# Kernel optimization log

Hardware: AMD Instinct MI355X
Metric: run time of the kernel (lower is better)

Reference implementation:

```python
import jax, jax.numpy as jnp
import numpy as np

IN_F = 512
OUT_F = 512
ALPHA = 0.2  # LeakyReLU negative slope
# dropout p=0.1 is a no-op at inference (training=False), so omitted


def setup_inputs() -> dict:
    key = jax.random.key(0)
    k1, k2, k3 = jax.random.split(key, 3)
    B, N = 16, 1024
    x = jax.random.normal(k1, (B, N, IN_F), dtype=jnp.float32)
    # xavier_uniform with gain=1.414
    limW = 1.414 * np.sqrt(6.0 / (IN_F + OUT_F))
    W = jax.random.uniform(k2, (IN_F, OUT_F), minval=-limW, maxval=limW, dtype=jnp.float32)
    lima = 1.414 * np.sqrt(6.0 / (2 * OUT_F + 1))
    a = jax.random.uniform(k3, (2 * OUT_F, 1), minval=-lima, maxval=lima, dtype=jnp.float32)
    beta = jnp.ones((1,), dtype=jnp.float32)
    return {"x": x, "W": W, "a": a, "beta": beta}


def reference(x, W, a, beta):
    # h: [B, N, F]
    h = jnp.matmul(x, W)
    # Split attention vector: e_ij = leakyrelu(h_i . a1 + h_j . a2)
    a1 = a[:OUT_F, 0]   # [F]
    a2 = a[OUT_F:, 0]   # [F]
    s1 = jnp.einsum('bnf,f->bn', h, a1)  # [B, N]
    s2 = jnp.einsum('bnf,f->bn', h, a2)  # [B, N]
    e = s1[:, :, None] + s2[:, None, :]  # [B, N, N]
    e = jnp.where(e > 0, e, ALPHA * e)   # LeakyReLU
    attention = jax.nn.softmax(e, axis=2)
    h_prime = jnp.einsum('bnm,bmf->bnf', attention, h)
    out = jax.nn.elu(h_prime + beta * h)
    return out
```

## Files before the change

kernel.cpp:

```cpp
#include <hip/hip_runtime.h>

using u16 = unsigned short;
using u32 = unsigned int;

#define ALPHA 0.2f
#define LOG2E 1.4426950408889634f

typedef __bf16 bf16x8 __attribute__((ext_vector_type(8)));
typedef float f32x4 __attribute__((ext_vector_type(4)));
typedef float f32x16 __attribute__((ext_vector_type(16)));

__device__ __forceinline__ u16 f2bf(float f) {
  u32 u = __builtin_bit_cast(u32, f);
  u += 0x7FFFu + ((u >> 16) & 1u);
  return (u16)(u >> 16);
}
__device__ __forceinline__ float bf2f(u16 h) {
  u32 u = ((u32)h) << 16;
  return __builtin_bit_cast(float, u);
}
__device__ __forceinline__ void gload_lds16(const void* g, void* l) {
  __builtin_amdgcn_global_load_lds((__attribute__((address_space(1))) void*)g,
                                   (__attribute__((address_space(3))) void*)l,
                                   16, 0, 0);
}

__global__ __launch_bounds__(256) void k_cast_wT(const float* __restrict__ W, u16* __restrict__ wbt) {
  int idx = blockIdx.x * 256 + threadIdx.x;
  int k = idx >> 9, n = idx & 511;
  wbt[n * 512 + k] = f2bf(W[idx]);
}


__global__ __launch_bounds__(256, 2) void k_gemm1(const float* __restrict__ x, const u16* __restrict__ wbt,
                                                  const float* __restrict__ a,
                                                  u16* __restrict__ hbf, u16* __restrict__ hbt2,
                                                  float* __restrict__ s1p, float* __restrict__ s2p) {
  __shared__ __attribute__((aligned(16))) char lds[73728];
  __shared__ __attribute__((aligned(16))) float a_l[256];

  const int t = threadIdx.x;
  const int lane = t & 63;
  const int w = t >> 6;
  const int l31 = lane & 31, lhi = lane >> 5;
  const int rb = w >> 1, cg = w & 1;
  const int g = blockIdx.x;
  const int cb = (g >> 3) & 3;
  const int tile_m = (g & 7) | ((g >> 5) << 3);
  const int row0 = tile_m * 128;
  const int col0 = cb * 128;

  a_l[t] = (t < 128) ? a[col0 + t] : a[512 + col0 + (t - 128)];

  f32x16 acc[2][2];
#pragma unroll
  for (int i = 0; i < 2; ++i)
#pragma unroll
    for (int j = 0; j < 2; ++j)
#pragma unroll
      for (int r = 0; r < 16; ++r) acc[i][j][r] = 0.f;

#define STAGE_G1(kt, Ab, Bb)                                                              \
  {                                                                                       \
    const int k0_ = (kt) * 32;                                                            \
    _Pragma("unroll")                                                                     \
    for (int i = 0; i < 4; ++i) {                                                         \
      int G = i * 256 + t;                                                                \
      int row = G >> 3, ks = G & 7;                                                       \
      gload_lds16(x + (size_t)(row0 + row) * 512 + k0_ + ((ks ^ (row & 7)) * 4),          \
                  (Ab) + (size_t)(i * 256 + w * 64) * 16);                                \
    }                                                                                     \
    _Pragma("unroll")                                                                     \
    for (int i = 0; i < 2; ++i) {                                                         \
      int G = i * 256 + t;                                                                \
      int col = G >> 2, ks = G & 3;                                                       \
      gload_lds16(wbt + (size_t)(col0 + col) * 512 + k0_ + ((ks ^ ((col >> 1) & 3)) * 8), \
                  (Bb) + (size_t)(i * 256 + w * 64) * 16);                                \
    }                                                                                     \
  }

#define COMPUTE_G1(Ab, Bb)                                                                         \
  {                                                                                                \
    _Pragma("unroll")                                                                              \
    for (int ks = 0; ks < 2; ++ks) {                                                               \
      bf16x8 af[2];                                                                                \
      _Pragma("unroll")                                                                            \
      for (int sub = 0; sub < 2; ++sub) {                                                          \
        const int arow = rb * 64 + sub * 32 + l31;                                                 \
        const int kg = ks * 4 + lhi * 2;                                                           \
        f32x4 fa0 = *reinterpret_cast<const f32x4*>((Ab) + (size_t)(arow * 8 + (kg ^ (arow & 7))) * 16); \
        f32x4 fa1 = *reinterpret_cast<const f32x4*>((Ab) + (size_t)(arow * 8 + ((kg + 1) ^ (arow & 7))) * 16); \
        _Pragma("unroll")                                                                          \
        for (int jj = 0; jj < 4; ++jj) {                                                           \
          af[sub][jj] = (__bf16)fa0[jj];                                                           \
          af[sub][jj + 4] = (__bf16)fa1[jj];                                                       \
        }                                                                                          \
      }                                                                                            \
      bf16x8 bfr[2];                                                                               \
      _Pragma("unroll")                                                                            \
      for (int bt = 0; bt < 2; ++bt) {                                                             \
        const int bcol = cg * 64 + bt * 32 + l31;                                                  \
        const int kslot = (ks * 2 + lhi) ^ ((bcol >> 1) & 3);                                      \
        bfr[bt] = *reinterpret_cast<const bf16x8*>((Bb) + (size_t)(bcol * 4 + kslot) * 16);        \
      }                                                                                            \
      _Pragma("unroll")                                                                            \
      for (int sub = 0; sub < 2; ++sub)                                                            \
        _Pragma("unroll")                                                                          \
        for (int bt = 0; bt < 2; ++bt)                                                             \
          acc[sub][bt] = __builtin_amdgcn_mfma_f32_32x32x16_bf16(af[sub], bfr[bt], acc[sub][bt], 0, 0, 0); \
    }                                                                                              \
  }

  char* Ac = lds;             char* Bc = lds + 49152;
  char* An = lds + 16384;     char* Bn = lds + 57344;
  char* As = lds + 32768;     char* Bs = lds + 65536;

  STAGE_G1(0, Ac, Bc);
  STAGE_G1(1, An, Bn);
  __builtin_amdgcn_sched_barrier(0);
  asm volatile("s_waitcnt vmcnt(6) lgkmcnt(0)" ::: "memory");
  __builtin_amdgcn_s_barrier();
  __builtin_amdgcn_sched_barrier(0);

#pragma unroll 1
  for (int kt = 0; kt < 14; ++kt) {
    STAGE_G1(kt + 2, As, Bs);
    COMPUTE_G1(Ac, Bc);
    __builtin_amdgcn_sched_barrier(0);
    asm volatile("s_waitcnt vmcnt(6)" ::: "memory");
    __builtin_amdgcn_s_barrier();
    __builtin_amdgcn_sched_barrier(0);
    char* ta = Ac; Ac = An; An = As; As = ta;
    char* tb = Bc; Bc = Bn; Bn = Bs; Bs = tb;
  }
  COMPUTE_G1(Ac, Bc);
  __builtin_amdgcn_sched_barrier(0);
  asm volatile("s_waitcnt vmcnt(0)" ::: "memory");
  __builtin_amdgcn_s_barrier();
  __builtin_amdgcn_sched_barrier(0);
  COMPUTE_G1(An, Bn);
#undef STAGE_G1
#undef COMPUTE_G1

  __syncthreads();

  u16* lT = (u16*)lds;
#pragma unroll
  for (int sub = 0; sub < 2; ++sub)
#pragma unroll
    for (int bt = 0; bt < 2; ++bt) {
      const int col = cg * 64 + bt * 32 + l31;
#pragma unroll
      for (int r = 0; r < 16; ++r) {
        int row = rb * 64 + sub * 32 + (r & 3) + 8 * (r >> 2) + 4 * lhi;
        lT[row * 136 + col] = f2bf(acc[sub][bt][r]);
      }
    }
  __syncthreads();

#pragma unroll
  for (int i = 0; i < 8; ++i) {
    int G = i * 256 + t;
    int row = G >> 4, gg = G & 15;
    uint4 v = *reinterpret_cast<const uint4*>(&lT[row * 136 + gg * 8]);
    *reinterpret_cast<uint4*>(&hbf[(size_t)(row0 + row) * 512 + col0 + gg * 8]) = v;
  }
  const int bb = row0 >> 10;
  const int nb = row0 & 1023;
  u16* hb2 = hbt2 + (size_t)bb * 524288;
#pragma unroll
  for (int i = 0; i < 8; ++i) {
    int G = i * 256 + t;
    int col = G & 127, rg = G >> 7;
    u32 wd[4];
#pragma unroll
    for (int jj = 0; jj < 4; ++jj) {
      u16 lo = lT[(rg * 8 + 2 * jj) * 136 + col];
      u16 hi = lT[(rg * 8 + 2 * jj + 1) * 136 + col];
      wd[jj] = (u32)lo | ((u32)hi << 16);
    }
    uint4 o = {wd[0], wd[1], wd[2], wd[3]};
    const int m0 = nb + rg * 8;
    const int f = col0 + col;
    size_t idx = (size_t)(m0 >> 4) * 8192 + (size_t)(f >> 5) * 512 + (size_t)((m0 >> 3) & 1) * 256 + (size_t)(f & 31) * 8;
    *reinterpret_cast<uint4*>(&hb2[idx]) = o;
  }
  {
    const int r2 = t >> 1, half = t & 1;
    float d1 = 0.f, d2 = 0.f;
#pragma unroll
    for (int i = 0; i < 8; ++i) {
      uint4 v = *reinterpret_cast<const uint4*>(&lT[r2 * 136 + half * 64 + i * 8]);
      u32 wds[4] = {v.x, v.y, v.z, v.w};
#pragma unroll
      for (int jj = 0; jj < 8; ++jj) {
        float h = bf2f((u16)(wds[jj >> 1] >> ((jj & 1) * 16)));
        d1 += h * a_l[half * 64 + i * 8 + jj];
        d2 += h * a_l[128 + half * 64 + i * 8 + jj];
      }
    }
    d1 += __shfl_xor(d1, 1);
    d2 += __shfl_xor(d2, 1);
    if (half == 0) {
      s1p[cb * 16384 + row0 + r2] = d1;
      s2p[cb * 16384 + row0 + r2] = d2;
    }
  }
}

__global__ __launch_bounds__(256) void k_reduce(const float* __restrict__ s1p, const float* __restrict__ s2p,
                                                float* __restrict__ s1L, float* __restrict__ s2L) {
  int id = blockIdx.x * 256 + threadIdx.x;
  float d1 = s1p[id] + s1p[16384 + id] + s1p[32768 + id] + s1p[49152 + id];
  float d2 = s2p[id] + s2p[16384 + id] + s2p[32768 + id] + s2p[49152 + id];
  s1L[id] = d1 * LOG2E;
  s2L[id] = d2 * LOG2E;
}

__global__ __launch_bounds__(256, 2) void k_attn(const u16* __restrict__ hbt2, const u16* __restrict__ hbf,
                                                 const float* __restrict__ s1Lg, const float* __restrict__ s2Lg,
                                                 const float* __restrict__ betag, float* __restrict__ out) {
  __shared__ __attribute__((aligned(16))) float e1_l[1024];
  __shared__ __attribute__((aligned(16))) float e2_l[1024];
  __shared__ __attribute__((aligned(16))) float inv_l[128];
  const int t = threadIdx.x;
  const int lane = t & 63;
  const int w = t >> 6;
  const int l31 = lane & 31, lhi = lane >> 5;

  const int B = blockIdx.x;
  const int b = (B & 7) * 2 + ((B >> 3) & 1);
  const int j = B >> 4;
  const int n0 = (j >> 2) * 128;
  const int c0 = (j & 3) * 128;

  const u16* hb2 = hbt2 + (size_t)b * 524288;

  for (int i = t; i < 1024; i += 256) {
    float v = s2Lg[b * 1024 + i];
    e1_l[i] = exp2f(v);
    e2_l[i] = exp2f(ALPHA * v);
  }

  const int myrow = n0 + w * 32 + l31;
  const float s1v = s1Lg[b * 1024 + myrow];
  const float c1 = exp2f(s1v), c2 = exp2f(ALPHA * s1v);

  f32x16 acc[4];
#pragma unroll
  for (int ct = 0; ct < 4; ++ct)
#pragma unroll
    for (int r = 0; r < 16; ++r) acc[ct][r] = 0.f;
  float psum = 0.f;

  __syncthreads();

  const u16* bp = hb2 + (size_t)(c0 >> 5) * 512 + (size_t)(lhi * 32 + l31) * 8;

#define STEP_ATTN(s, buf)                                                      \
  {                                                                            \
    const int mo = (s) * 16 + lhi * 8;                                         \
    f32x4 ea = *reinterpret_cast<const f32x4*>(&e1_l[mo]);                     \
    f32x4 eb = *reinterpret_cast<const f32x4*>(&e1_l[mo + 4]);                 \
    f32x4 fa = *reinterpret_cast<const f32x4*>(&e2_l[mo]);                     \
    f32x4 fb = *reinterpret_cast<const f32x4*>(&e2_l[mo + 4]);                 \
    bf16x8 af;                                                                 \
    _Pragma("unroll")                                                          \
    for (int q = 0; q < 4; ++q) {                                              \
      float p0 = fmaxf(c1 * ea[q], c2 * fa[q]);                                \
      float p1 = fmaxf(c1 * eb[q], c2 * fb[q]);                                \
      psum += p0 + p1;                                                         \
      af[q] = (__bf16)p0;                                                      \
      af[q + 4] = (__bf16)p1;                                                  \
    }                                                                          \
    _Pragma("unroll")                                                          \
    for (int ct = 0; ct < 4; ++ct)                                             \
      acc[ct] = __builtin_amdgcn_mfma_f32_32x32x16_bf16(af, (buf)[ct], acc[ct], 0, 0, 0); \
  }

  bf16x8 bv[4];
#pragma unroll
  for (int ct = 0; ct < 4; ++ct) bv[ct] = *reinterpret_cast<const bf16x8*>(bp + ct * 512);

#pragma unroll 4
  for (int s = 0; s < 63; ++s) {
    bf16x8 nv[4];
    const u16* np = bp + (size_t)(s + 1) * 8192;
#pragma unroll
    for (int ct = 0; ct < 4; ++ct) nv[ct] = *reinterpret_cast<const bf16x8*>(np + ct * 512);
    STEP_ATTN(s, bv);
#pragma unroll
    for (int ct = 0; ct < 4; ++ct) bv[ct] = nv[ct];
  }
  STEP_ATTN(63, bv);
#undef STEP_ATTN

  psum += __shfl_xor(psum, 32);
  if (lhi == 0) inv_l[w * 32 + l31] = 1.0f / psum;
  __syncthreads();

  const float beta = betag[0];
  const u16* hf = hbf + (size_t)b * 1024 * 512;
#pragma unroll
  for (int ct = 0; ct < 4; ++ct) {
    const int colv = c0 + ct * 32 + l31;
#pragma unroll
    for (int rg = 0; rg < 4; ++rg) {
      const int rl = rg * 8 + lhi * 4;
      const int rowb = n0 + w * 32 + rl;
      f32x4 iv = *reinterpret_cast<const f32x4*>(&inv_l[w * 32 + rl]);
#pragma unroll
      for (int q = 0; q < 4; ++q) {
        float hv = bf2f(hf[(size_t)(rowb + q) * 512 + colv]);
        float xv = acc[ct][rg * 4 + q] * iv[q] + beta * hv;
        out[((size_t)b * 1024 + rowb + q) * 512 + colv] = xv > 0.f ? xv : __expf(xv) - 1.0f;
      }
    }
  }
}

extern "C" void kernel_launch(void* const* d_in, const int* in_sizes, int n_in,
                              void* d_out, int out_size, void* d_ws, size_t ws_size,
                              hipStream_t stream) {
  const float* x = (const float*)d_in[0];
  const float* W = (const float*)d_in[1];
  const float* a = (const float*)d_in[2];
  const float* beta = (const float*)d_in[3];
  float* out = (float*)d_out;

  char* ws = (char*)d_ws;
  u16* hbf = (u16*)ws;
  u16* hbt2 = (u16*)(ws + (16u << 20));
  u16* wbt = (u16*)(ws + (32u << 20));
  float* s1p = (float*)(ws + (32u << 20) + (512u << 10));
  float* s2p = (float*)(ws + (32u << 20) + (768u << 10));
  float* s1L = (float*)(ws + (33u << 20));
  float* s2L = (float*)(ws + (33u << 20) + (64u << 10));

  k_cast_wT<<<1024, 256, 0, stream>>>(W, wbt);
  k_gemm1<<<512, 256, 0, stream>>>(x, wbt, a, hbf, hbt2, s1p, s2p);
  k_reduce<<<64, 256, 0, stream>>>(s1p, s2p, s1L, s2L);
  k_attn<<<512, 256, 0, stream>>>(hbt2, hbf, s1L, s2L, beta, out);
}
```

Baseline: 71.51 us.

## Compute softmax row sums via MFMA with ones and deepen B-operand prefetch

Replaces the scalar per-lane psum accumulation plus shuffle, LDS store and barrier with an extra MFMA against a ones vector, so each row's denominator lands directly in the accumulator layout. It also replaces the one-step double-buffered global loads with an 8-deep register rotation of B fragments, giving more loads in flight to hide latency. The costs are one extra MFMA per step (about 25% more matrix work) and much higher register pressure from 32 prefetched bf16x8 vectors, which could lower occupancy below the two blocks per CU requested by the launch bounds. The denominator is now summed from bf16-rounded probabilities, which slightly changes numerics.

After: 67.16 us. -6.1%, faster.

```diff
diff --git a/kernel.cpp b/kernel.cpp
--- a/kernel.cpp
+++ b/kernel.cpp
@@ -222,7 +222,6 @@
                                                  const float* __restrict__ betag, float* __restrict__ out) {
   __shared__ __attribute__((aligned(16))) float e1_l[1024];
   __shared__ __attribute__((aligned(16))) float e2_l[1024];
-  __shared__ __attribute__((aligned(16))) float inv_l[128];
   const int t = threadIdx.x;
   const int lane = t & 63;
   const int w = t >> 6;
@@ -251,11 +250,23 @@
   for (int ct = 0; ct < 4; ++ct)
 #pragma unroll
     for (int r = 0; r < 16; ++r) acc[ct][r] = 0.f;
-  float psum = 0.f;
+  f32x16 accs;
+#pragma unroll
+  for (int r = 0; r < 16; ++r) accs[r] = 0.f;
+  bf16x8 ones;
+#pragma unroll
+  for (int q = 0; q < 8; ++q) ones[q] = (__bf16)1.0f;
 
   __syncthreads();
 
   const u16* bp = hb2 + (size_t)(c0 >> 5) * 512 + (size_t)(lhi * 32 + l31) * 8;
+
+#define LOAD_B(dst, s)                                                                         \
+  {                                                                                            \
+    const u16* np_ = bp + (size_t)(s) * 8192;                                                  \
+    _Pragma("unroll")                                                                          \
+    for (int ct = 0; ct < 4; ++ct) dst[ct] = *reinterpret_cast<const bf16x8*>(np_ + ct * 512); \
+  }
 
 #define STEP_ATTN(s, buf)                                                      \
   {                                                                            \
@@ -267,48 +278,46 @@
     bf16x8 af;                                                                 \
     _Pragma("unroll")                                                          \
     for (int q = 0; q < 4; ++q) {                                              \
-      float p0 = fmaxf(c1 * ea[q], c2 * fa[q]);                                \
-      float p1 = fmaxf(c1 * eb[q], c2 * fb[q]);                                \
-      psum += p0 + p1;                                                         \
-      af[q] = (__bf16)p0;                                                      \
-      af[q + 4] = (__bf16)p1;                                                  \
+      af[q] = (__bf16)fmaxf(c1 * ea[q], c2 * fa[q]);                           \
+      af[q + 4] = (__bf16)fmaxf(c1 * eb[q], c2 * fb[q]);                       \
     }                                                                          \
+    accs = __builtin_amdgcn_mfma_f32_32x32x16_bf16(af, ones, accs, 0, 0, 0);   \
     _Pragma("unroll")                                                          \
     for (int ct = 0; ct < 4; ++ct)                                             \
       acc[ct] = __builtin_amdgcn_mfma_f32_32x32x16_bf16(af, (buf)[ct], acc[ct], 0, 0, 0); \
   }
 
-  bf16x8 bv[4];
-#pragma unroll
-  for (int ct = 0; ct < 4; ++ct) bv[ct] = *reinterpret_cast<const bf16x8*>(bp + ct * 512);
-
-#pragma unroll 4
-  for (int s = 0; s < 63; ++s) {
-    bf16x8 nv[4];
-    const u16* np = bp + (size_t)(s + 1) * 8192;
-#pragma unroll
-    for (int ct = 0; ct < 4; ++ct) nv[ct] = *reinterpret_cast<const bf16x8*>(np + ct * 512);
-    STEP_ATTN(s, bv);
-#pragma unroll
-    for (int ct = 0; ct < 4; ++ct) bv[ct] = nv[ct];
-  }
-  STEP_ATTN(63, bv);
+  bf16x8 P0[4], P1[4], P2[4], P3[4], P4[4], P5[4], P6[4], P7[4];
+  LOAD_B(P0, 0); LOAD_B(P1, 1); LOAD_B(P2, 2); LOAD_B(P3, 3);
+  LOAD_B(P4, 4); LOAD_B(P5, 5); LOAD_B(P6, 6); LOAD_B(P7, 7);
+
+#pragma unroll 1
+  for (int s = 0; s < 56; s += 8) {
+    STEP_ATTN(s + 0, P0); LOAD_B(P0, s + 8);
+    STEP_ATTN(s + 1, P1); LOAD_B(P1, s + 9);
+    STEP_ATTN(s + 2, P2); LOAD_B(P2, s + 10);
+    STEP_ATTN(s + 3, P3); LOAD_B(P3, s + 11);
+    STEP_ATTN(s + 4, P4); LOAD_B(P4, s + 12);
+    STEP_ATTN(s + 5, P5); LOAD_B(P5, s + 13);
+    STEP_ATTN(s + 6, P6); LOAD_B(P6, s + 14);
+    STEP_ATTN(s + 7, P7); LOAD_B(P7, s + 15);
+  }
+  STEP_ATTN(56, P0); STEP_ATTN(57, P1); STEP_ATTN(58, P2); STEP_ATTN(59, P3);
+  STEP_ATTN(60, P4); STEP_ATTN(61, P5); STEP_ATTN(62, P6); STEP_ATTN(63, P7);
+#undef LOAD_B
 #undef STEP_ATTN
-
-  psum += __shfl_xor(psum, 32);
-  if (lhi == 0) inv_l[w * 32 + l31] = 1.0f / psum;
-  __syncthreads();
 
   const float beta = betag[0];
   const u16* hf = hbf + (size_t)b * 1024 * 512;
 #pragma unroll
-  for (int ct = 0; ct < 4; ++ct) {
-    const int colv = c0 + ct * 32 + l31;
-#pragma unroll
-    for (int rg = 0; rg < 4; ++rg) {
-      const int rl = rg * 8 + lhi * 4;
-      const int rowb = n0 + w * 32 + rl;
-      f32x4 iv = *reinterpret_cast<const f32x4*>(&inv_l[w * 32 + rl]);
+  for (int rg = 0; rg < 4; ++rg) {
+    f32x4 iv;
+#pragma unroll
+    for (int q = 0; q < 4; ++q) iv[q] = 1.0f / accs[rg * 4 + q];
+#pragma unroll
+    for (int ct = 0; ct < 4; ++ct) {
+      const int colv = c0 + ct * 32 + l31;
+      const int rowb = n0 + w * 32 + rg * 8 + lhi * 4;
 #pragma unroll
       for (int q = 0; q < 4; ++q) {
         float hv = bf2f(hf[(size_t)(rowb + q) * 512 + colv]);
```

## Replace dense attention matmul with sorted prefix-sum formulation of rank-one LeakyReLU softmax

Applied to the files above, without the earlier changes.

Uses the fact that exp(leakyrelu(s1_i+s2_j)) splits into two exponential branches depending on whether s2_j exceeds -s1_i. Each batch's s2 values are sorted, the split point per row is found by binary search, and h_prime becomes a weighted prefix or suffix sum of h rows in sorted order. This removes the N×N×F matmul, replacing it with a bitonic sort kernel, a sequential prefix-sweep kernel that writes a per-row table, and an elementwise final kernel. The cost is serial dependency in the sweep, gathered loads, extra launches and a large intermediate table stored in bf16.

New measurement: 209.4 us. 2.93x slower.

```diff
diff --git a/kernel.cpp b/kernel.cpp
--- a/kernel.cpp
+++ b/kernel.cpp
@@ -2,6 +2,7 @@
 
 using u16 = unsigned short;
 using u32 = unsigned int;
+using u64 = unsigned long long;
 
 #define ALPHA 0.2f
 #define LOG2E 1.4426950408889634f
@@ -31,10 +32,9 @@
   wbt[n * 512 + k] = f2bf(W[idx]);
 }
 
-
 __global__ __launch_bounds__(256, 2) void k_gemm1(const float* __restrict__ x, const u16* __restrict__ wbt,
                                                   const float* __restrict__ a,
-                                                  u16* __restrict__ hbf, u16* __restrict__ hbt2,
+                                                  u16* __restrict__ hbf,
                                                   float* __restrict__ s1p, float* __restrict__ s2p) {
   __shared__ __attribute__((aligned(16))) char lds[73728];
   __shared__ __attribute__((aligned(16))) float a_l[256];
@@ -165,26 +165,6 @@
     uint4 v = *reinterpret_cast<const uint4*>(&lT[row * 136 + gg * 8]);
     *reinterpret_cast<uint4*>(&hbf[(size_t)(row0 + row) * 512 + col0 + gg * 8]) = v;
   }
-  const int bb = row0 >> 10;
-  const int nb = row0 & 1023;
-  u16* hb2 = hbt2 + (size_t)bb * 524288;
-#pragma unroll
-  for (int i = 0; i < 8; ++i) {
-    int G = i * 256 + t;
-    int col = G & 127, rg = G >> 7;
-    u32 wd[4];
-#pragma unroll
-    for (int jj = 0; jj < 4; ++jj) {
-      u16 lo = lT[(rg * 8 + 2 * jj) * 136 + col];
-      u16 hi = lT[(rg * 8 + 2 * jj + 1) * 136 + col];
-      wd[jj] = (u32)lo | ((u32)hi << 16);
-    }
-    uint4 o = {wd[0], wd[1], wd[2], wd[3]};
-    const int m0 = nb + rg * 8;
-    const int f = col0 + col;
-    size_t idx = (size_t)(m0 >> 4) * 8192 + (size_t)(f >> 5) * 512 + (size_t)((m0 >> 3) & 1) * 256 + (size_t)(f & 31) * 8;
-    *reinterpret_cast<uint4*>(&hb2[idx]) = o;
-  }
   {
     const int r2 = t >> 1, half = t & 1;
     float d1 = 0.f, d2 = 0.f;
@@ -217,106 +197,212 @@
   s2L[id] = d2 * LOG2E;
 }
 
-__global__ __launch_bounds__(256, 2) void k_attn(const u16* __restrict__ hbt2, const u16* __restrict__ hbf,
-                                                 const float* __restrict__ s1Lg, const float* __restrict__ s2Lg,
-                                                 const float* __restrict__ betag, float* __restrict__ out) {
-  __shared__ __attribute__((aligned(16))) float e1_l[1024];
-  __shared__ __attribute__((aligned(16))) float e2_l[1024];
-  __shared__ __attribute__((aligned(16))) float inv_l[128];
+__global__ __launch_bounds__(1024) void k_prep(const float* __restrict__ s1Lg, const float* __restrict__ s2Lg,
+                                               float* __restrict__ e1s, float* __restrict__ e2s,
+                                               u32* __restrict__ permM, u32* __restrict__ krows,
+                                               float* __restrict__ invd) {
+  __shared__ u64 sk[1024];
+  __shared__ float s2sv[1024];
+  __shared__ float arrA[1024];
+  __shared__ float arrB[1024];
+  const int b = blockIdx.x;
+  const int t = threadIdx.x;
+
+  {
+    float v = s2Lg[b * 1024 + t];
+    u32 bits = __builtin_bit_cast(u32, v);
+    u32 key = (bits & 0x80000000u) ? ~bits : (bits | 0x80000000u);
+    sk[t] = ((u64)key << 32) | (u32)t;
+  }
+  for (int size = 2; size <= 1024; size <<= 1)
+    for (int stride = size >> 1; stride > 0; stride >>= 1) {
+      __syncthreads();
+      int ixj = t ^ stride;
+      if (ixj > t) {
+        u64 va = sk[t], vb = sk[ixj];
+        bool asc = ((t & size) == 0);
+        if ((va > vb) == asc) { sk[t] = vb; sk[ixj] = va; }
+      }
+    }
+  __syncthreads();
+
+  const u32 idx = (u32)(sk[t] & 1023u);
+  const float sv = s2Lg[b * 1024 + idx];
+  s2sv[t] = sv;
+  __syncthreads();
+
+  const float E1 = exp2f(sv), E2 = exp2f(ALPHA * sv);
+  e1s[b * 1024 + t] = E1;
+  e2s[b * 1024 + t] = E2;
+  permM[b * 1024 + t] = idx;
+  arrA[t] = E2;
+  arrB[t] = exp2f(s2sv[1023 - t]);
+  __syncthreads();
+
+  for (int off = 1; off < 1024; off <<= 1) {
+    float aA = (t >= off) ? arrA[t - off] : 0.f;
+    float aB = (t >= off) ? arrB[t - off] : 0.f;
+    __syncthreads();
+    arrA[t] += aA;
+    arrB[t] += aB;
+    __syncthreads();
+  }
+
+  int kn;
+  {
+    const float s1v = s1Lg[b * 1024 + t];
+    const float thr = -s1v;
+    int lo = 0, hi = 1024;
+    while (lo < hi) { int mid = (lo + hi) >> 1; if (s2sv[mid] <= thr) lo = mid + 1; else hi = mid; }
+    kn = lo;
+    float se1suf = (kn == 1024) ? 0.f : arrB[1023 - kn];
+    float se2pre = (kn == 0) ? 0.f : arrA[kn - 1];
+    float den = exp2f(s1v) * se1suf + exp2f(ALPHA * s1v) * se2pre;
+    invd[b * 1024 + t] = 1.0f / den;
+  }
+
+  u32* sk32 = (u32*)sk;
+  __syncthreads();
+  sk32[t] = ((u32)kn << 10) | (u32)t;
+  for (int size = 2; size <= 1024; size <<= 1)
+    for (int stride = size >> 1; stride > 0; stride >>= 1) {
+      __syncthreads();
+      int ixj = t ^ stride;
+      if (ixj > t) {
+        u32 va = sk32[t], vb = sk32[ixj];
+        bool asc = ((t & size) == 0);
+        if ((va > vb) == asc) { sk32[t] = vb; sk32[ixj] = va; }
+      }
+    }
+  __syncthreads();
+  krows[b * 1024 + t] = sk32[t];
+}
+
+__global__ __launch_bounds__(256, 2) void k_sweep(const u16* __restrict__ hbf,
+                                                  const float* __restrict__ e1s, const float* __restrict__ e2s,
+                                                  const u32* __restrict__ permM, const u32* __restrict__ krows,
+                                                  u32* __restrict__ tab) {
+  __shared__ u32 krows_l[1024];
+  __shared__ float e1_l[1024];
+  __shared__ float e2_l[1024];
+  __shared__ u32 perm_l[1024];
+  __shared__ float T1[4][64];
+  __shared__ float T2[4][64];
+
+  const int t = threadIdx.x;
+  const int lane = t & 63;
+  const int mg = t >> 6;
+  const int B = blockIdx.x;
+  const int b = (B & 7) * 2 + ((B >> 3) & 1);
+  const int j2 = B >> 4;
+  const int fc = j2 >> 2;
+  const int nq = j2 & 3;
+  const int nhLo = nq * 256, nhHi = nhLo + 256;
+  const int fcol = fc * 64 + lane;
+
+#pragma unroll
+  for (int q = 0; q < 4; ++q) {
+    int i = q * 256 + t;
+    krows_l[i] = krows[b * 1024 + i];
+    e1_l[i] = e1s[b * 1024 + i];
+    e2_l[i] = e2s[b * 1024 + i];
+    perm_l[i] = permM[b * 1024 + i];
+  }
+  __syncthreads();
+
+  const int lo = mg * 256;
+  float t1 = 0.f, t2 = 0.f;
+#pragma unroll 2
+  for (int ii = 0; ii < 256; ++ii) {
+    int i = lo + ii;
+    float hv = bf2f(hbf[(size_t)(b * 1024 + perm_l[i]) * 512 + fcol]);
+    t1 = fmaf(e1_l[i], hv, t1);
+    t2 = fmaf(e2_l[i], hv, t2);
+  }
+  T1[mg][lane] = t1;
+  T2[mg][lane] = t2;
+  __syncthreads();
+
+  float base1 = 0.f, base2 = 0.f, tot2 = 0.f;
+#pragma unroll
+  for (int m2 = 0; m2 < 4; ++m2) {
+    float v2 = T2[m2][lane];
+    tot2 += v2;
+    if (m2 > mg) { base1 += T1[m2][lane]; base2 += v2; }
+  }
+
+  int ptr;
+  {
+    const int kin = lo + 256;
+    int l2 = 0, h2 = 1024;
+    while (l2 < h2) { int mid = (l2 + h2) >> 1; if ((int)(krows_l[mid] >> 10) <= kin) l2 = mid + 1; else h2 = mid; }
+    ptr = l2 < nhHi ? l2 : nhHi;
+  }
+
+  float acc1 = base1, acc2 = base2;
+  u32* tabb = tab + (size_t)b * 1024 * 512 + fcol;
+#pragma unroll 1
+  for (int ii = 255; ii >= 0; --ii) {
+    const int i = lo + ii;
+    const int k = i + 1;
+    while (ptr > nhLo) {
+      u32 v = krows_l[ptr - 1];
+      if ((int)(v >> 10) != k) break;
+      u32 pk = (u32)f2bf(acc1) | ((u32)f2bf(tot2 - acc2) << 16);
+      tabb[(size_t)(ptr - 1) * 512] = pk;
+      --ptr;
+    }
+    float hv = bf2f(hbf[(size_t)(b * 1024 + perm_l[i]) * 512 + fcol]);
+    acc1 = fmaf(e1_l[i], hv, acc1);
+    acc2 = fmaf(e2_l[i], hv, acc2);
+  }
+  if (mg == 0) {
+    while (ptr > nhLo && (krows_l[ptr - 1] >> 10) == 0) {
+      u32 pk = (u32)f2bf(acc1) | ((u32)f2bf(tot2 - acc2) << 16);
+      tabb[(size_t)(ptr - 1) * 512] = pk;
+      --ptr;
+    }
+  }
+}
+
+__global__ __launch_bounds__(256) void k_final(const u32* __restrict__ tab, const u32* __restrict__ krows,
+                                               const float* __restrict__ s1Lg, const float* __restrict__ invd,
+                                               const u16* __restrict__ hbf, const float* __restrict__ betag,
+                                               float* __restrict__ out) {
   const int t = threadIdx.x;
   const int lane = t & 63;
   const int w = t >> 6;
-  const int l31 = lane & 31, lhi = lane >> 5;
-
-  const int B = blockIdx.x;
-  const int b = (B & 7) * 2 + ((B >> 3) & 1);
-  const int j = B >> 4;
-  const int n0 = (j >> 2) * 128;
-  const int c0 = (j & 3) * 128;
-
-  const u16* hb2 = hbt2 + (size_t)b * 524288;
-
-  for (int i = t; i < 1024; i += 256) {
-    float v = s2Lg[b * 1024 + i];
-    e1_l[i] = exp2f(v);
-    e2_l[i] = exp2f(ALPHA * v);
-  }
-
-  const int myrow = n0 + w * 32 + l31;
-  const float s1v = s1Lg[b * 1024 + myrow];
+  const int gid = blockIdx.x;
+  const int b = (gid & 7) * 2 + ((gid >> 3) & 1);
+  const int rg = gid >> 4;
+  const int j = rg * 4 + w;
+
+  const u32 kr = krows[b * 1024 + j];
+  const int n = kr & 1023;
+  const float s1v = s1Lg[b * 1024 + n];
   const float c1 = exp2f(s1v), c2 = exp2f(ALPHA * s1v);
-
-  f32x16 acc[4];
-#pragma unroll
-  for (int ct = 0; ct < 4; ++ct)
-#pragma unroll
-    for (int r = 0; r < 16; ++r) acc[ct][r] = 0.f;
-  float psum = 0.f;
-
-  __syncthreads();
-
-  const u16* bp = hb2 + (size_t)(c0 >> 5) * 512 + (size_t)(lhi * 32 + l31) * 8;
-
-#define STEP_ATTN(s, buf)                                                      \
-  {                                                                            \
-    const int mo = (s) * 16 + lhi * 8;                                         \
-    f32x4 ea = *reinterpret_cast<const f32x4*>(&e1_l[mo]);                     \
-    f32x4 eb = *reinterpret_cast<const f32x4*>(&e1_l[mo + 4]);                 \
-    f32x4 fa = *reinterpret_cast<const f32x4*>(&e2_l[mo]);                     \
-    f32x4 fb = *reinterpret_cast<const f32x4*>(&e2_l[mo + 4]);                 \
-    bf16x8 af;                                                                 \
-    _Pragma("unroll")                                                          \
-    for (int q = 0; q < 4; ++q) {                                              \
-      float p0 = fmaxf(c1 * ea[q], c2 * fa[q]);                                \
-      float p1 = fmaxf(c1 * eb[q], c2 * fb[q]);                                \
-      psum += p0 + p1;                                                         \
-      af[q] = (__bf16)p0;                                                      \
-      af[q + 4] = (__bf16)p1;                                                  \
-    }                                                                          \
-    _Pragma("unroll")                                                          \
-    for (int ct = 0; ct < 4; ++ct)                                             \
-      acc[ct] = __builtin_amdgcn_mfma_f32_32x32x16_bf16(af, (buf)[ct], acc[ct], 0, 0, 0); \
-  }
-
-  bf16x8 bv[4];
-#pragma unroll
-  for (int ct = 0; ct < 4; ++ct) bv[ct] = *reinterpret_cast<const bf16x8*>(bp + ct * 512);
-
-#pragma unroll 4
-  for (int s = 0; s < 63; ++s) {
-    bf16x8 nv[4];
-    const u16* np = bp + (size_t)(s + 1) * 8192;
-#pragma unroll
-    for (int ct = 0; ct < 4; ++ct) nv[ct] = *reinterpret_cast<const bf16x8*>(np + ct * 512);
-    STEP_ATTN(s, bv);
-#pragma unroll
-    for (int ct = 0; ct < 4; ++ct) bv[ct] = nv[ct];
-  }
-  STEP_ATTN(63, bv);
-#undef STEP_ATTN
-
-  psum += __shfl_xor(psum, 32);
-  if (lhi == 0) inv_l[w * 32 + l31] = 1.0f / psum;
-  __syncthreads();
-
+  const float inv = invd[b * 1024 + n];
   const float beta = betag[0];
-  const u16* hf = hbf + (size_t)b * 1024 * 512;
-#pragma unroll
-  for (int ct = 0; ct < 4; ++ct) {
-    const int colv = c0 + ct * 32 + l31;
-#pragma unroll
-    for (int rg = 0; rg < 4; ++rg) {
-      const int rl = rg * 8 + lhi * 4;
-      const int rowb = n0 + w * 32 + rl;
-      f32x4 iv = *reinterpret_cast<const f32x4*>(&inv_l[w * 32 + rl]);
-#pragma unroll
-      for (int q = 0; q < 4; ++q) {
-        float hv = bf2f(hf[(size_t)(rowb + q) * 512 + colv]);
-        float xv = acc[ct][rg * 4 + q] * iv[q] + beta * hv;
-        out[((size_t)b * 1024 + rowb + q) * 512 + colv] = xv > 0.f ? xv : __expf(xv) - 1.0f;
-      }
-    }
-  }
+
+  const u32* trow = tab + ((size_t)b * 1024 + j) * 512 + lane * 8;
+  uint4 ta = reinterpret_cast<const uint4*>(trow)[0];
+  uint4 tb2 = reinterpret_cast<const uint4*>(trow)[1];
+  uint4 hv4 = *reinterpret_cast<const uint4*>(hbf + ((size_t)b * 1024 + n) * 512 + lane * 8);
+
+  u32 tw[8] = {ta.x, ta.y, ta.z, ta.w, tb2.x, tb2.y, tb2.z, tb2.w};
+  u32 hw[4] = {hv4.x, hv4.y, hv4.z, hv4.w};
+  float res[8];
+#pragma unroll
+  for (int q = 0; q < 8; ++q) {
+    float A = bf2f((u16)(tw[q] & 0xFFFFu));
+    float Bv = bf2f((u16)(tw[q] >> 16));
+    float hvf = bf2f((u16)(hw[q >> 1] >> ((q & 1) * 16)));
+    float xv = (c1 * A + c2 * Bv) * inv + beta * hvf;
+    res[q] = xv > 0.f ? xv : __expf(xv) - 1.0f;
+  }
+  float* op = out + ((size_t)b * 1024 + n) * 512 + lane * 8;
+  reinterpret_cast<float4*>(op)[0] = make_float4(res[0], res[1], res[2], res[3]);
+  reinterpret_cast<float4*>(op)[1] = make_float4(res[4], res[5], res[6], res[7]);
 }
 
 extern "C" void kernel_launch(void* const* d_in, const int* in_sizes, int n_in,
@@ -330,15 +416,23 @@
 
   char* ws = (char*)d_ws;
   u16* hbf = (u16*)ws;
-  u16* hbt2 = (u16*)(ws + (16u << 20));
-  u16* wbt = (u16*)(ws + (32u << 20));
-  float* s1p = (float*)(ws + (32u << 20) + (512u << 10));
-  float* s2p = (float*)(ws + (32u << 20) + (768u << 10));
-  float* s1L = (float*)(ws + (33u << 20));
-  float* s2L = (float*)(ws + (33u << 20) + (64u << 10));
+  u32* tab = (u32*)(ws + (16u << 20));
+  char* sm = ws + (50u << 20);
+  float* e1s = (float*)(sm);
+  float* e2s = (float*)(sm + (64u << 10));
+  u32* permM = (u32*)(sm + (128u << 10));
+  u32* krows = (u32*)(sm + (192u << 10));
+  float* invd = (float*)(sm + (256u << 10));
+  float* s1L = (float*)(sm + (320u << 10));
+  float* s2L = (float*)(sm + (384u << 10));
+  float* s1p = (float*)(sm + (448u << 10));
+  float* s2p = (float*)(sm + (704u << 10));
+  u16* wbt = (u16*)(ws + (51u << 20));
 
   k_cast_wT<<<1024, 256, 0, stream>>>(W, wbt);
-  k_gemm1<<<512, 256, 0, stream>>>(x, wbt, a, hbf, hbt2, s1p, s2p);
+  k_gemm1<<<512, 256, 0, stream>>>(x, wbt, a, hbf, s1p, s2p);
   k_reduce<<<64, 256, 0, stream>>>(s1p, s2p, s1L, s2L);
-  k_attn<<<512, 256, 0, stream>>>(hbt2, hbf, s1L, s2L, beta, out);
-}
+  k_prep<<<16, 1024, 0, stream>>>(s1L, s2L, e1s, e2s, permM, krows, invd);
+  k_sweep<<<512, 256, 0, stream>>>(hbf, e1s, e2s, permM, krows, tab);
+  k_final<<<4096, 256, 0, stream>>>(tab, krows, s1L, invd, hbf, beta, out);
+}
```
